# Performance work log

Hardware: AMD Instinct MI355X
Metric: run time of the kernel (lower is better)

The kernel has to match this reference:

```python
import jax, jax.numpy as jnp
import numpy as np

IN_C, HID_C, OUT_C = 128, 256, 128
N_NODES, N_EDGES = 50000, 600000


def setup_inputs() -> dict:
    key = jax.random.key(0)
    ks = jax.random.split(key, 8)
    x = jax.random.normal(ks[0], (N_NODES, IN_C), dtype=jnp.float32)
    edge_index = jax.random.randint(ks[1], (2, N_EDGES), 0, N_NODES, dtype=jnp.int64)
    def glorot(k, shape):
        lim = np.sqrt(6.0 / (shape[0] + shape[1])).astype(np.float32)
        return jax.random.uniform(k, shape, dtype=jnp.float32, minval=-lim, maxval=lim)
    # PyG SAGEConv: out = lin_l(mean_aggr) + lin_r(x_root); bias only in lin_l
    W1_l = glorot(ks[2], (IN_C, HID_C)); b1 = jnp.zeros((HID_C,), jnp.float32)
    W1_r = glorot(ks[3], (IN_C, HID_C))
    W2_l = glorot(ks[4], (HID_C, OUT_C)); b2 = jnp.zeros((OUT_C,), jnp.float32)
    W2_r = glorot(ks[5], (HID_C, OUT_C))
    return {"x": x, "edge_index": edge_index, "W1_l": W1_l, "b1": b1, "W1_r": W1_r,
            "W2_l": W2_l, "b2": b2, "W2_r": W2_r}


def _sage_conv(x, src, dst, W_l, b, W_r):
    n = x.shape[0]
    msg = x[src]  # [E, C] gather from source nodes
    agg = jax.ops.segment_sum(msg, dst, num_segments=n)
    cnt = jax.ops.segment_sum(jnp.ones((src.shape[0],), x.dtype), dst, num_segments=n)
    agg = agg / jnp.maximum(cnt, 1.0)[:, None]  # mean aggregation, zero-deg safe
    return agg @ W_l + b + x @ W_r


def reference(x, edge_index, W1_l, b1, W1_r, W2_l, b2, W2_r):
    src, dst = edge_index[0], edge_index[1]
    h = jax.nn.relu(_sage_conv(x, src, dst, W1_l, b1, W1_r))
    return _sage_conv(h, src, dst, W2_l, b2, W2_r)
```

## Files before the change

kernel.cpp:

```cpp
#include <hip/hip_runtime.h>
#include <hip/hip_bf16.h>


#define N_NODES 50000
#define IN_C    128
#define HID_C   256
#define OUT_C   128
#define N_EDGES 600000
#define SLOTS   64

#define PB_FILL 586
#define PB_W1   (PB_FILL + 256)
#define PB_W2   (PB_W1 + 256)
#define PB_X    (PB_W2 + 6250)

typedef __attribute__((ext_vector_type(8))) short short8;
typedef __attribute__((ext_vector_type(8))) unsigned short ushort8;
typedef __attribute__((ext_vector_type(4))) unsigned short ushort4u;
typedef __attribute__((ext_vector_type(4))) float f32x4;
typedef __attribute__((ext_vector_type(2))) float f32x2;

__device__ __forceinline__ float bf2f(short s) {
    union { unsigned u; float f; } c;
    c.u = ((unsigned)(unsigned short)s) << 16;
    return c.f;
}
__device__ __forceinline__ unsigned f2fp8(float v) {
    return (unsigned)__builtin_amdgcn_cvt_pk_fp8_f32(v, v, 0, false) & 0xffu;
}
__device__ __forceinline__ void acc_fp8x4(float* a, unsigned u) {
    f32x2 lo = __builtin_amdgcn_cvt_pk_f32_fp8(u, false);
    f32x2 hi = __builtin_amdgcn_cvt_pk_f32_fp8(u, true);
    a[0] += lo[0]; a[1] += lo[1]; a[2] += hi[0]; a[3] += hi[1];
}

__global__ __launch_bounds__(256) void prep(
    const float* __restrict__ x, __hip_bfloat16* __restrict__ xbf,
    const float* __restrict__ W1l, const float* __restrict__ W1r,
    const float* __restrict__ W2l, const float* __restrict__ W2r,
    __hip_bfloat16* __restrict__ W1t, __hip_bfloat16* __restrict__ W2t,
    const int* __restrict__ srcI, const int* __restrict__ dstI,
    int* __restrict__ cur, unsigned short* __restrict__ colp) {
    int b = blockIdx.x;
    if (b < PB_FILL) {
        int base = b * 1024 + threadIdx.x;
        #pragma unroll
        for (int k = 0; k < 4; ++k) {
            int e = base + k * 256;
            if (e < N_EDGES) {
                int d = dstI[e];
                int pos = atomicAdd(&cur[d], 1);
                if (pos < SLOTS)
                    __builtin_nontemporal_store(
                        (unsigned short)srcI[e], &colp[(size_t)d * SLOTS + pos]);
            }
        }
    } else if (b < PB_W1) {
        int reg = b - PB_FILL;
        int half = reg >> 7;
        int t = (reg & 127) * 256 + threadIdx.x;
        int k = t >> 8, n = t & 255;
        const float* src = half ? W1r : W1l;
        W1t[n * 256 + half * 128 + k] = __float2bfloat16(src[t]);
    } else if (b < PB_W2) {
        int reg = b - PB_W1;
        int half = reg >> 7;
        int t = (reg & 127) * 256 + threadIdx.x;
        int k = t >> 7, n = t & 127;
        const float* src = half ? W2r : W2l;
        W2t[(size_t)(half * 128 + n) * 256 + k] = __float2bfloat16(src[t]);
    } else {
        int t = (b - PB_W2) * 256 + threadIdx.x;
        if (t >= N_NODES * 32) return;
        int row = t >> 5, c = (t & 31) * 4;
        float4 v = *(const float4*)(x + (size_t)row * 128 + c);
        __hip_bfloat16* d = xbf + (size_t)row * 128 + c;
        __hip_bfloat162 p0, p1;
        p0.x = __float2bfloat16(v.x); p0.y = __float2bfloat16(v.y);
        p1.x = __float2bfloat16(v.z); p1.y = __float2bfloat16(v.w);
        *(__hip_bfloat162*)d = p0;
        *(__hip_bfloat162*)(d + 2) = p1;
    }
}

__global__ __launch_bounds__(256, 4) void fused_fwd(
    const __hip_bfloat16* __restrict__ xbf,
    const int* __restrict__ deg, const unsigned short* __restrict__ colp,
    const __hip_bfloat16* __restrict__ W1t,
    const float* __restrict__ b1,
    const __hip_bfloat16* __restrict__ W2t,
    const float* __restrict__ b2,
    unsigned char* __restrict__ hp,
    float* __restrict__ pre,
    int M) {
    __shared__ __hip_bfloat16 hAB[64 * 256];

    int tid  = threadIdx.x;
    int wave = tid >> 6, lane = tid & 63;
    int mb   = blockIdx.x * 64;
    int sl   = tid & 15;

    for (int pass = 0; pass < 4; ++pass) {
        int r = pass * 16 + (tid >> 4);
        int node = mb + r; if (node >= M) node = M - 1;
        int d = deg[node]; if (d > SLOTS) d = SLOTS;
        const unsigned short* col = colp + (size_t)node * SLOTS;
        const __hip_bfloat16* base = xbf + sl * 8;
        float a[8];
        #pragma unroll
        for (int c = 0; c < 8; ++c) a[c] = 0.f;

        int j = 0;
        if (d >= 8) {
            ushort8 ci = __builtin_nontemporal_load((const ushort8*)col);
            short8 v0 = *(const short8*)(base + (size_t)ci[0] * 128);
            short8 v1 = *(const short8*)(base + (size_t)ci[1] * 128);
            short8 v2 = *(const short8*)(base + (size_t)ci[2] * 128);
            short8 v3 = *(const short8*)(base + (size_t)ci[3] * 128);
            short8 v4 = *(const short8*)(base + (size_t)ci[4] * 128);
            short8 v5 = *(const short8*)(base + (size_t)ci[5] * 128);
            short8 v6 = *(const short8*)(base + (size_t)ci[6] * 128);
            short8 v7 = *(const short8*)(base + (size_t)ci[7] * 128);
            for (; j + 16 <= d; j += 8) {
                ushort8 cx = __builtin_nontemporal_load(
                                 (const ushort8*)(col + j + 8));
                short8 w0 = *(const short8*)(base + (size_t)cx[0] * 128);
                short8 w1 = *(const short8*)(base + (size_t)cx[1] * 128);
                short8 w2 = *(const short8*)(base + (size_t)cx[2] * 128);
                short8 w3 = *(const short8*)(base + (size_t)cx[3] * 128);
                short8 w4 = *(const short8*)(base + (size_t)cx[4] * 128);
                short8 w5 = *(const short8*)(base + (size_t)cx[5] * 128);
                short8 w6 = *(const short8*)(base + (size_t)cx[6] * 128);
                short8 w7 = *(const short8*)(base + (size_t)cx[7] * 128);
                #pragma unroll
                for (int c = 0; c < 8; ++c)
                    a[c] += (bf2f(v0[c]) + bf2f(v1[c])) + (bf2f(v2[c]) + bf2f(v3[c]));
                #pragma unroll
                for (int c = 0; c < 8; ++c)
                    a[c] += (bf2f(v4[c]) + bf2f(v5[c])) + (bf2f(v6[c]) + bf2f(v7[c]));
                v0 = w0; v1 = w1; v2 = w2; v3 = w3;
                v4 = w4; v5 = w5; v6 = w6; v7 = w7;
            }
            #pragma unroll
            for (int c = 0; c < 8; ++c)
                a[c] += (bf2f(v0[c]) + bf2f(v1[c])) + (bf2f(v2[c]) + bf2f(v3[c]));
            #pragma unroll
            for (int c = 0; c < 8; ++c)
                a[c] += (bf2f(v4[c]) + bf2f(v5[c])) + (bf2f(v6[c]) + bf2f(v7[c]));
            j += 8;
        }
        if (d - j >= 4) {
            ushort4u c4 = __builtin_nontemporal_load((const ushort4u*)(col + j));
            short8 v0 = *(const short8*)(base + (size_t)c4[0] * 128);
            short8 v1 = *(const short8*)(base + (size_t)c4[1] * 128);
            short8 v2 = *(const short8*)(base + (size_t)c4[2] * 128);
            short8 v3 = *(const short8*)(base + (size_t)c4[3] * 128);
            #pragma unroll
            for (int c = 0; c < 8; ++c)
                a[c] += (bf2f(v0[c]) + bf2f(v1[c])) + (bf2f(v2[c]) + bf2f(v3[c]));
            j += 4;
        }
        int rem = d - j;
        if (rem > 0) {
            int s0 = col[j];
            int s1 = (rem > 1) ? col[j + 1] : s0;
            int s2 = (rem > 2) ? col[j + 2] : s0;
            short8 t0 = *(const short8*)(base + (size_t)s0 * 128);
            short8 t1 = *(const short8*)(base + (size_t)s1 * 128);
            short8 t2 = *(const short8*)(base + (size_t)s2 * 128);
            #pragma unroll
            for (int c = 0; c < 8; ++c) a[c] += bf2f(t0[c]);
            if (rem > 1) {
                #pragma unroll
                for (int c = 0; c < 8; ++c) a[c] += bf2f(t1[c]);
            }
            if (rem > 2) {
                #pragma unroll
                for (int c = 0; c < 8; ++c) a[c] += bf2f(t2[c]);
            }
        }

        float inv = 1.f / (float)max(d, 1);
        short8 q;
        #pragma unroll
        for (int c = 0; c < 8; ++c) {
            union { __hip_bfloat16 b; short s; } cv;
            cv.b = __float2bfloat16(a[c] * inv);
            q[c] = cv.s;
        }
        int pc = (sl & 8) | ((sl & 7) ^ (r & 7));
        *(short8*)&hAB[r * 256 + pc * 8] = q;
        short8 sv = *(const short8*)(xbf + (size_t)node * 128 + sl * 8);
        *(short8*)&hAB[r * 256 + (16 + pc) * 8] = sv;
    }
    __syncthreads();

    f32x4 acc[4][4];
    #pragma unroll
    for (int i = 0; i < 4; ++i)
        #pragma unroll
        for (int j = 0; j < 4; ++j)
            acc[i][j] = (f32x4){0.f, 0.f, 0.f, 0.f};

    for (int kt = 0; kt < 256; kt += 64) {
        #pragma unroll
        for (int ks = 0; ks < 64; ks += 32) {
            int chunkL = (ks >> 3) + (lane >> 4);
            short8 af[4], bf[4];
            #pragma unroll
            for (int j = 0; j < 4; ++j) {
                int brow = wave * 64 + j * 16 + (lane & 15);
                bf[j] = *(const short8*)(W1t + (size_t)brow * 256 + kt + ks
                                         + (lane >> 4) * 8);
            }
            #pragma unroll
            for (int i = 0; i < 4; ++i) {
                int row = i * 16 + (lane & 15);
                af[i] = *(const short8*)&hAB[row * 256 +
                        ((kt >> 3) + (chunkL ^ (row & 7))) * 8];
            }
            #pragma unroll
            for (int i = 0; i < 4; ++i)
                #pragma unroll
                for (int j = 0; j < 4; ++j)
                    acc[i][j] = __builtin_amdgcn_mfma_f32_16x16x32_bf16(
                        af[i], bf[j], acc[i][j], 0, 0, 0);
        }
    }
    __syncthreads();

    int cn[4];
    float bc[4];
    #pragma unroll
    for (int j = 0; j < 4; ++j) {
        cn[j] = wave * 64 + j * 16 + (lane & 15);
        bc[j] = b1[cn[j]];
    }
    #pragma unroll
    for (int i = 0; i < 4; ++i)
        #pragma unroll
        for (int r = 0; r < 4; ++r) {
            int row = i * 16 + (lane >> 4) * 4 + r;
            #pragma unroll
            for (int j = 0; j < 4; ++j) {
                float v = fmaxf(acc[i][j][r] + bc[j], 0.f);
                int c = cn[j] >> 3;
                int pchk = (c & ~7) | ((c & 7) ^ (row & 7));
                union { __hip_bfloat16 b; short s; } cv;
                cv.b = __float2bfloat16(v);
                *(short*)&hAB[row * 256 + pchk * 8 + (cn[j] & 7)] = cv.s;
            }
        }
    __syncthreads();

    #pragma unroll
    for (int i = 0; i < 4; ++i)
        #pragma unroll
        for (int j = 0; j < 4; ++j)
            acc[i][j] = (f32x4){0.f, 0.f, 0.f, 0.f};

    for (int kt = 0; kt < 256; kt += 64) {
        #pragma unroll
        for (int ks = 0; ks < 64; ks += 32) {
            int chunkL = (ks >> 3) + (lane >> 4);
            short8 af[4], bf[4];
            #pragma unroll
            for (int j = 0; j < 4; ++j) {
                int brow = wave * 64 + j * 16 + (lane & 15);
                bf[j] = *(const short8*)(W2t + (size_t)brow * 256 + kt + ks
                                         + (lane >> 4) * 8);
            }
            #pragma unroll
            for (int i = 0; i < 4; ++i) {
                int row = i * 16 + (lane & 15);
                af[i] = *(const short8*)&hAB[row * 256 +
                        ((kt >> 3) + (chunkL ^ (row & 7))) * 8];
            }
            #pragma unroll
            for (int i = 0; i < 4; ++i)
                #pragma unroll
                for (int j = 0; j < 4; ++j)
                    acc[i][j] = __builtin_amdgcn_mfma_f32_16x16x32_bf16(
                        af[i], bf[j], acc[i][j], 0, 0, 0);
        }
    }

    if (wave < 2) {
        #pragma unroll
        for (int i = 0; i < 4; ++i)
            #pragma unroll
            for (int r = 0; r < 4; ++r) {
                int row = mb + i * 16 + (lane >> 4) * 4 + r;
                if (row >= M) continue;
                #pragma unroll
                for (int j = 0; j < 4; ++j)
                    hp[(size_t)row * 128 + cn[j]] = (unsigned char)f2fp8(acc[i][j][r]);
            }
    } else {
        float bc2[4];
        #pragma unroll
        for (int j = 0; j < 4; ++j) bc2[j] = b2[cn[j] - 128];
        #pragma unroll
        for (int i = 0; i < 4; ++i)
            #pragma unroll
            for (int r = 0; r < 4; ++r) {
                int row = mb + i * 16 + (lane >> 4) * 4 + r;
                if (row >= M) continue;
                #pragma unroll
                for (int j = 0; j < 4; ++j)
                    __builtin_nontemporal_store(
                        acc[i][j][r] + bc2[j],
                        &pre[(size_t)row * 128 + cn[j] - 128]);
            }
    }
}

__global__ __launch_bounds__(256) void aggregate_fp8_final(
    const unsigned char* __restrict__ feat,
    const int* __restrict__ deg, const unsigned short* __restrict__ colp,
    float* __restrict__ outp, const float* __restrict__ pre, int nNodes) {
    int node = blockIdx.x * 16 + (threadIdx.x >> 4);
    int sl   = threadIdx.x & 15;
    if (node >= nNodes) return;
    int d   = deg[node]; if (d > SLOTS) d = SLOTS;
    const unsigned short* col = colp + (size_t)node * SLOTS;
    const unsigned char* base = feat + sl * 8;
    float a[8];
    #pragma unroll
    for (int c = 0; c < 8; ++c) a[c] = 0.f;

    int j = 0;
    if (d >= 8) {
        ushort8 ci = __builtin_nontemporal_load((const ushort8*)col);
        uint2 v0 = *(const uint2*)(base + (size_t)ci[0] * 128);
        uint2 v1 = *(const uint2*)(base + (size_t)ci[1] * 128);
        uint2 v2 = *(const uint2*)(base + (size_t)ci[2] * 128);
        uint2 v3 = *(const uint2*)(base + (size_t)ci[3] * 128);
        uint2 v4 = *(const uint2*)(base + (size_t)ci[4] * 128);
        uint2 v5 = *(const uint2*)(base + (size_t)ci[5] * 128);
        uint2 v6 = *(const uint2*)(base + (size_t)ci[6] * 128);
        uint2 v7 = *(const uint2*)(base + (size_t)ci[7] * 128);
        for (; j + 16 <= d; j += 8) {
            ushort8 cx = __builtin_nontemporal_load((const ushort8*)(col + j + 8));
            uint2 w0 = *(const uint2*)(base + (size_t)cx[0] * 128);
            uint2 w1 = *(const uint2*)(base + (size_t)cx[1] * 128);
            uint2 w2 = *(const uint2*)(base + (size_t)cx[2] * 128);
            uint2 w3 = *(const uint2*)(base + (size_t)cx[3] * 128);
            uint2 w4 = *(const uint2*)(base + (size_t)cx[4] * 128);
            uint2 w5 = *(const uint2*)(base + (size_t)cx[5] * 128);
            uint2 w6 = *(const uint2*)(base + (size_t)cx[6] * 128);
            uint2 w7 = *(const uint2*)(base + (size_t)cx[7] * 128);
            acc_fp8x4(a,     v0.x); acc_fp8x4(a,     v1.x);
            acc_fp8x4(a,     v2.x); acc_fp8x4(a,     v3.x);
            acc_fp8x4(a + 4, v0.y); acc_fp8x4(a + 4, v1.y);
            acc_fp8x4(a + 4, v2.y); acc_fp8x4(a + 4, v3.y);
            acc_fp8x4(a,     v4.x); acc_fp8x4(a,     v5.x);
            acc_fp8x4(a,     v6.x); acc_fp8x4(a,     v7.x);
            acc_fp8x4(a + 4, v4.y); acc_fp8x4(a + 4, v5.y);
            acc_fp8x4(a + 4, v6.y); acc_fp8x4(a + 4, v7.y);
            v0 = w0; v1 = w1; v2 = w2; v3 = w3;
            v4 = w4; v5 = w5; v6 = w6; v7 = w7;
        }
        acc_fp8x4(a,     v0.x); acc_fp8x4(a,     v1.x);
        acc_fp8x4(a,     v2.x); acc_fp8x4(a,     v3.x);
        acc_fp8x4(a + 4, v0.y); acc_fp8x4(a + 4, v1.y);
        acc_fp8x4(a + 4, v2.y); acc_fp8x4(a + 4, v3.y);
        acc_fp8x4(a,     v4.x); acc_fp8x4(a,     v5.x);
        acc_fp8x4(a,     v6.x); acc_fp8x4(a,     v7.x);
        acc_fp8x4(a + 4, v4.y); acc_fp8x4(a + 4, v5.y);
        acc_fp8x4(a + 4, v6.y); acc_fp8x4(a + 4, v7.y);
        j += 8;
    }
    if (d - j >= 4) {
        ushort4u c4 = __builtin_nontemporal_load((const ushort4u*)(col + j));
        uint2 v0 = *(const uint2*)(base + (size_t)c4[0] * 128);
        uint2 v1 = *(const uint2*)(base + (size_t)c4[1] * 128);
        uint2 v2 = *(const uint2*)(base + (size_t)c4[2] * 128);
        uint2 v3 = *(const uint2*)(base + (size_t)c4[3] * 128);
        acc_fp8x4(a,     v0.x); acc_fp8x4(a,     v1.x);
        acc_fp8x4(a,     v2.x); acc_fp8x4(a,     v3.x);
        acc_fp8x4(a + 4, v0.y); acc_fp8x4(a + 4, v1.y);
        acc_fp8x4(a + 4, v2.y); acc_fp8x4(a + 4, v3.y);
        j += 4;
    }
    for (; j < d; ++j) {
        uint2 v = *(const uint2*)(base + (size_t)col[j] * 128);
        acc_fp8x4(a, v.x);
        acc_fp8x4(a + 4, v.y);
    }

    float inv = 1.f / (float)max(d, 1);
    const f32x4* pp = (const f32x4*)(pre + (size_t)node * 128 + sl * 8);
    f32x4 p0 = __builtin_nontemporal_load(pp);
    f32x4 p1 = __builtin_nontemporal_load(pp + 1);
    f32x4 o0 = {a[0] * inv + p0[0], a[1] * inv + p0[1],
                a[2] * inv + p0[2], a[3] * inv + p0[3]};
    f32x4 o1 = {a[4] * inv + p1[0], a[5] * inv + p1[1],
                a[6] * inv + p1[2], a[7] * inv + p1[3]};
    f32x4* op = (f32x4*)(outp + (size_t)node * 128 + sl * 8);
    __builtin_nontemporal_store(o0, op);
    __builtin_nontemporal_store(o1, op + 1);
}

extern "C" void kernel_launch(void* const* d_in, const int* in_sizes, int n_in,
                              void* d_out, int out_size, void* d_ws, size_t ws_size,
                              hipStream_t stream) {
    const float* x    = (const float*)d_in[0];
    const int*   ei   = (const int*)d_in[1];
    const float* W1l  = (const float*)d_in[2];
    const float* b1   = (const float*)d_in[3];
    const float* W1r  = (const float*)d_in[4];
    const float* W2l  = (const float*)d_in[5];
    const float* b2   = (const float*)d_in[6];
    const float* W2r  = (const float*)d_in[7];
    float* out = (float*)d_out;

    const int N = N_NODES;
    const int* srcI = ei;
    const int* dstI = ei + N_EDGES;

    char* w = (char*)d_ws;
    int*             cur   = (int*)(w + 0);
    unsigned short*  colp  = (unsigned short*)(w + 204800);
    __hip_bfloat16*  W1t   = (__hip_bfloat16*)(w + 6604800);
    __hip_bfloat16*  W2t   = (__hip_bfloat16*)(w + 6735872);
    __hip_bfloat16*  xbf   = (__hip_bfloat16*)(w + 6866944);
    unsigned char*   hp_f8 = (unsigned char*)(w + 19666944);
    float*           pre   = (float*)(w + 26066944);

    hipMemsetAsync(cur, 0, 200000, stream);
    prep<<<PB_X, 256, 0, stream>>>(x, xbf, W1l, W1r, W2l, W2r, W1t, W2t,
                                   srcI, dstI, cur, colp);

    fused_fwd<<<(N + 63) / 64, 256, 0, stream>>>(
        xbf, cur, colp, W1t, b1, W2t, b2, hp_f8, pre, N);

    aggregate_fp8_final<<<(N + 15) / 16, 256, 0, stream>>>(
        hp_f8, cur, colp, out, pre, N);
}
```

Measured before the change: 201.0 us.

## Halve fused tile rows, raise occupancy, drop nontemporal hints, widen fill blocks

```diff
diff --git a/kernel.cpp b/kernel.cpp
--- a/kernel.cpp
+++ b/kernel.cpp
@@ -8,8 +8,9 @@
 #define OUT_C   128
 #define N_EDGES 600000
 #define SLOTS   64
-
-#define PB_FILL 586
+#define FROWS   32
+
+#define PB_FILL 293
 #define PB_W1   (PB_FILL + 256)
 #define PB_W2   (PB_W1 + 256)
 #define PB_X    (PB_W2 + 6250)
@@ -43,16 +44,15 @@
     int* __restrict__ cur, unsigned short* __restrict__ colp) {
     int b = blockIdx.x;
     if (b < PB_FILL) {
-        int base = b * 1024 + threadIdx.x;
-        #pragma unroll
-        for (int k = 0; k < 4; ++k) {
+        int base = b * 2048 + threadIdx.x;
+        #pragma unroll
+        for (int k = 0; k < 8; ++k) {
             int e = base + k * 256;
             if (e < N_EDGES) {
                 int d = dstI[e];
                 int pos = atomicAdd(&cur[d], 1);
                 if (pos < SLOTS)
-                    __builtin_nontemporal_store(
-                        (unsigned short)srcI[e], &colp[(size_t)d * SLOTS + pos]);
+                    colp[(size_t)d * SLOTS + pos] = (unsigned short)srcI[e];
             }
         }
     } else if (b < PB_W1) {
@@ -83,7 +83,7 @@
     }
 }
 
-__global__ __launch_bounds__(256, 4) void fused_fwd(
+__global__ __launch_bounds__(256, 6) void fused_fwd(
     const __hip_bfloat16* __restrict__ xbf,
     const int* __restrict__ deg, const unsigned short* __restrict__ colp,
     const __hip_bfloat16* __restrict__ W1t,
@@ -93,14 +93,14 @@
     unsigned char* __restrict__ hp,
     float* __restrict__ pre,
     int M) {
-    __shared__ __hip_bfloat16 hAB[64 * 256];
+    __shared__ __hip_bfloat16 hAB[FROWS * 256];
 
     int tid  = threadIdx.x;
     int wave = tid >> 6, lane = tid & 63;
-    int mb   = blockIdx.x * 64;
+    int mb   = blockIdx.x * FROWS;
     int sl   = tid & 15;
 
-    for (int pass = 0; pass < 4; ++pass) {
+    for (int pass = 0; pass < 2; ++pass) {
         int r = pass * 16 + (tid >> 4);
         int node = mb + r; if (node >= M) node = M - 1;
         int d = deg[node]; if (d > SLOTS) d = SLOTS;
@@ -112,7 +112,7 @@
 
         int j = 0;
         if (d >= 8) {
-            ushort8 ci = __builtin_nontemporal_load((const ushort8*)col);
+            ushort8 ci = *(const ushort8*)col;
             short8 v0 = *(const short8*)(base + (size_t)ci[0] * 128);
             short8 v1 = *(const short8*)(base + (size_t)ci[1] * 128);
             short8 v2 = *(const short8*)(base + (size_t)ci[2] * 128);
@@ -122,8 +122,7 @@
             short8 v6 = *(const short8*)(base + (size_t)ci[6] * 128);
             short8 v7 = *(const short8*)(base + (size_t)ci[7] * 128);
             for (; j + 16 <= d; j += 8) {
-                ushort8 cx = __builtin_nontemporal_load(
-                                 (const ushort8*)(col + j + 8));
+                ushort8 cx = *(const ushort8*)(col + j + 8);
                 short8 w0 = *(const short8*)(base + (size_t)cx[0] * 128);
                 short8 w1 = *(const short8*)(base + (size_t)cx[1] * 128);
                 short8 w2 = *(const short8*)(base + (size_t)cx[2] * 128);
@@ -150,7 +149,7 @@
             j += 8;
         }
         if (d - j >= 4) {
-            ushort4u c4 = __builtin_nontemporal_load((const ushort4u*)(col + j));
+            ushort4u c4 = *(const ushort4u*)(col + j);
             short8 v0 = *(const short8*)(base + (size_t)c4[0] * 128);
             short8 v1 = *(const short8*)(base + (size_t)c4[1] * 128);
             short8 v2 = *(const short8*)(base + (size_t)c4[2] * 128);
@@ -195,9 +194,9 @@
     }
     __syncthreads();
 
-    f32x4 acc[4][4];
+    f32x4 acc[2][4];
     #pragma unroll
-    for (int i = 0; i < 4; ++i)
+    for (int i = 0; i < 2; ++i)
         #pragma unroll
         for (int j = 0; j < 4; ++j)
             acc[i][j] = (f32x4){0.f, 0.f, 0.f, 0.f};
@@ -206,7 +205,7 @@
         #pragma unroll
         for (int ks = 0; ks < 64; ks += 32) {
             int chunkL = (ks >> 3) + (lane >> 4);
-            short8 af[4], bf[4];
+            short8 af[2], bf[4];
             #pragma unroll
             for (int j = 0; j < 4; ++j) {
                 int brow = wave * 64 + j * 16 + (lane & 15);
@@ -214,13 +213,13 @@
                                          + (lane >> 4) * 8);
             }
             #pragma unroll
-            for (int i = 0; i < 4; ++i) {
+            for (int i = 0; i < 2; ++i) {
                 int row = i * 16 + (lane & 15);
                 af[i] = *(const short8*)&hAB[row * 256 +
                         ((kt >> 3) + (chunkL ^ (row & 7))) * 8];
             }
             #pragma unroll
-            for (int i = 0; i < 4; ++i)
+            for (int i = 0; i < 2; ++i)
                 #pragma unroll
                 for (int j = 0; j < 4; ++j)
                     acc[i][j] = __builtin_amdgcn_mfma_f32_16x16x32_bf16(
@@ -237,7 +236,7 @@
         bc[j] = b1[cn[j]];
     }
     #pragma unroll
-    for (int i = 0; i < 4; ++i)
+    for (int i = 0; i < 2; ++i)
         #pragma unroll
         for (int r = 0; r < 4; ++r) {
             int row = i * 16 + (lane >> 4) * 4 + r;
@@ -254,7 +253,7 @@
     __syncthreads();
 
     #pragma unroll
-    for (int i = 0; i < 4; ++i)
+    for (int i = 0; i < 2; ++i)
         #pragma unroll
         for (int j = 0; j < 4; ++j)
             acc[i][j] = (f32x4){0.f, 0.f, 0.f, 0.f};
@@ -263,7 +262,7 @@
         #pragma unroll
         for (int ks = 0; ks < 64; ks += 32) {
             int chunkL = (ks >> 3) + (lane >> 4);
-            short8 af[4], bf[4];
+            short8 af[2], bf[4];
             #pragma unroll
             for (int j = 0; j < 4; ++j) {
                 int brow = wave * 64 + j * 16 + (lane & 15);
@@ -271,13 +270,13 @@
                                          + (lane >> 4) * 8);
             }
             #pragma unroll
-            for (int i = 0; i < 4; ++i) {
+            for (int i = 0; i < 2; ++i) {
                 int row = i * 16 + (lane & 15);
                 af[i] = *(const short8*)&hAB[row * 256 +
                         ((kt >> 3) + (chunkL ^ (row & 7))) * 8];
             }
             #pragma unroll
-            for (int i = 0; i < 4; ++i)
+            for (int i = 0; i < 2; ++i)
                 #pragma unroll
                 for (int j = 0; j < 4; ++j)
                     acc[i][j] = __builtin_amdgcn_mfma_f32_16x16x32_bf16(
@@ -287,7 +286,7 @@
 
     if (wave < 2) {
         #pragma unroll
-        for (int i = 0; i < 4; ++i)
+        for (int i = 0; i < 2; ++i)
             #pragma unroll
             for (int r = 0; r < 4; ++r) {
                 int row = mb + i * 16 + (lane >> 4) * 4 + r;
@@ -301,16 +300,14 @@
         #pragma unroll
         for (int j = 0; j < 4; ++j) bc2[j] = b2[cn[j] - 128];
         #pragma unroll
-        for (int i = 0; i < 4; ++i)
+        for (int i = 0; i < 2; ++i)
             #pragma unroll
             for (int r = 0; r < 4; ++r) {
                 int row = mb + i * 16 + (lane >> 4) * 4 + r;
                 if (row >= M) continue;
                 #pragma unroll
                 for (int j = 0; j < 4; ++j)
-                    __builtin_nontemporal_store(
-                        acc[i][j][r] + bc2[j],
-                        &pre[(size_t)row * 128 + cn[j] - 128]);
+                    pre[(size_t)row * 128 + cn[j] - 128] = acc[i][j][r] + bc2[j];
             }
     }
 }
@@ -331,7 +328,7 @@
 
     int j = 0;
     if (d >= 8) {
-        ushort8 ci = __builtin_nontemporal_load((const ushort8*)col);
+        ushort8 ci = *(const ushort8*)col;
         uint2 v0 = *(const uint2*)(base + (size_t)ci[0] * 128);
         uint2 v1 = *(const uint2*)(base + (size_t)ci[1] * 128);
         uint2 v2 = *(const uint2*)(base + (size_t)ci[2] * 128);
@@ -341,7 +338,7 @@
         uint2 v6 = *(const uint2*)(base + (size_t)ci[6] * 128);
         uint2 v7 = *(const uint2*)(base + (size_t)ci[7] * 128);
         for (; j + 16 <= d; j += 8) {
-            ushort8 cx = __builtin_nontemporal_load((const ushort8*)(col + j + 8));
+            ushort8 cx = *(const ushort8*)(col + j + 8);
             uint2 w0 = *(const uint2*)(base + (size_t)cx[0] * 128);
             uint2 w1 = *(const uint2*)(base + (size_t)cx[1] * 128);
             uint2 w2 = *(const uint2*)(base + (size_t)cx[2] * 128);
@@ -372,7 +369,7 @@
         j += 8;
     }
     if (d - j >= 4) {
-        ushort4u c4 = __builtin_nontemporal_load((const ushort4u*)(col + j));
+        ushort4u c4 = *(const ushort4u*)(col + j);
         uint2 v0 = *(const uint2*)(base + (size_t)c4[0] * 128);
         uint2 v1 = *(const uint2*)(base + (size_t)c4[1] * 128);
         uint2 v2 = *(const uint2*)(base + (size_t)c4[2] * 128);
@@ -390,16 +387,14 @@
     }
 
     float inv = 1.f / (float)max(d, 1);
-    const f32x4* pp = (const f32x4*)(pre + (size_t)node * 128 + sl * 8);
-    f32x4 p0 = __builtin_nontemporal_load(pp);
-    f32x4 p1 = __builtin_nontemporal_load(pp + 1);
-    f32x4 o0 = {a[0] * inv + p0[0], a[1] * inv + p0[1],
-                a[2] * inv + p0[2], a[3] * inv + p0[3]};
-    f32x4 o1 = {a[4] * inv + p1[0], a[5] * inv + p1[1],
-                a[6] * inv + p1[2], a[7] * inv + p1[3]};
-    f32x4* op = (f32x4*)(outp + (size_t)node * 128 + sl * 8);
-    __builtin_nontemporal_store(o0, op);
-    __builtin_nontemporal_store(o1, op + 1);
+    const float* pp = pre + (size_t)node * 128 + sl * 8;
+    float* op = outp + (size_t)node * 128 + sl * 8;
+    float4 p0 = *(const float4*)pp;
+    float4 p1 = *(const float4*)(pp + 4);
+    *(float4*)op       = make_float4(a[0] * inv + p0.x, a[1] * inv + p0.y,
+                                     a[2] * inv + p0.z, a[3] * inv + p0.w);
+    *(float4*)(op + 4) = make_float4(a[4] * inv + p1.x, a[5] * inv + p1.y,
+                                     a[6] * inv + p1.z, a[7] * inv + p1.w);
 }
 
 extern "C" void kernel_launch(void* const* d_in, const int* in_sizes, int n_in,
@@ -432,7 +427,7 @@
     prep<<<PB_X, 256, 0, stream>>>(x, xbf, W1l, W1r, W2l, W2r, W1t, W2t,
                                    srcI, dstI, cur, colp);
 
-    fused_fwd<<<(N + 63) / 64, 256, 0, stream>>>(
+    fused_fwd<<<(N + FROWS - 1) / FROWS, 256, 0, stream>>>(
         xbf, cur, colp, W1t, b1, W2t, b2, hp_f8, pre, N);
 
     aggregate_fp8_final<<<(N + 15) / 16, 256, 0, stream>>>(
```

After: 224.7 us. 11.8% more time.
